# Performance work log

Measured on AMD Instinct MI355X. Metric: run time of the kernel, lower is better.

The kernel has to match this reference:

```python
import jax, jax.numpy as jnp
import numpy as np
import math

HEAD_SIZE = 64

def setup_inputs() -> dict:
    key = jax.random.key(0)
    k0, k1, k2, k3 = jax.random.split(key, 4)
    B, T, E, H = 4, 4096, 1024, HEAD_SIZE
    return {
        "x": jax.random.normal(k0, (B, T, E), dtype=jnp.float32),
        "Wq": jax.random.normal(k1, (E, H), dtype=jnp.float32) * (1.0 / math.sqrt(E)),
        "Wk": jax.random.normal(k2, (E, H), dtype=jnp.float32) * (1.0 / math.sqrt(E)),
        "Wv": jax.random.normal(k3, (E, H), dtype=jnp.float32) * (1.0 / math.sqrt(E)),
    }

def reference(x, Wq, Wk, Wv):
    # Single-head attention; faithful to source: softmax FIRST, then divide by sqrt(head_size)
    T = x.shape[-2]
    q = x @ Wq  # [B,T,H]
    k = x @ Wk
    v = x @ Wv
    scores = jnp.einsum('bth,bsh->bts', q, k)  # [B,T,T]
    # 'encoder' mask in this repo = lower-triangular (causal)
    causal = jnp.tril(jnp.ones((T, T), dtype=bool))
    scores = jnp.where(causal, scores, -jnp.inf)
    attn = jax.nn.softmax(scores, axis=-1) / jnp.sqrt(jnp.float32(q.shape[-1]))
    return jnp.einsum('bts,bsh->bth', attn, v)
```

## Files before the change

### kernel.cpp

```cpp
#include <hip/hip_runtime.h>
#include <math.h>

#define BB 4
#define TT 4096
#define EE 1024
#define HH 64

typedef __attribute__((ext_vector_type(8))) short bf16x8;
typedef _Float16 f16x8 __attribute__((ext_vector_type(8)));
typedef __attribute__((ext_vector_type(4))) float f32x4;

#define MFMA16(a, b, c)  __builtin_amdgcn_mfma_f32_16x16x32_bf16(a, b, c, 0, 0, 0)
#define MFMA16F(a, b, c) __builtin_amdgcn_mfma_f32_16x16x32_f16(a, b, c, 0, 0, 0)

__device__ __forceinline__ unsigned short f2bf_rne(float f) {
    unsigned u = __float_as_uint(f);
    unsigned r = u + 0x7fffu + ((u >> 16) & 1u);
    return (unsigned short)(r >> 16);
}
__device__ __forceinline__ float bf2f(unsigned short h) {
    return __uint_as_float(((unsigned)h) << 16);
}
__device__ __forceinline__ unsigned short f2h(float f) {
    union { _Float16 h; unsigned short u; } cv;
    cv.h = (_Float16)f;
    return cv.u;
}

__device__ __forceinline__ void async_copy16(const void* g, void* l) {
    __builtin_amdgcn_global_load_lds(
        (const __attribute__((address_space(1))) void*)g,
        (__attribute__((address_space(3))) void*)l, 16, 0, 0);
}
template<int N>
__device__ __forceinline__ void wait_vm() {
    __builtin_amdgcn_s_waitcnt(0x0f70 | (N & 15) | ((N >> 4) << 14));
}

__global__ __launch_bounds__(256) void wprep_kernel(
    const float* __restrict__ Wq, const float* __restrict__ Wk,
    const float* __restrict__ Wv,
    unsigned short* __restrict__ wt_hi, unsigned short* __restrict__ wt_lo)
{
    __shared__ float ts[64][65];
    const int which = blockIdx.x >> 4;
    const int e0 = (blockIdx.x & 15) * 64;
    const float* W = (which == 0) ? Wq : ((which == 1) ? Wk : Wv);
    const int t = threadIdx.x;
    const int h = t & 63;
    #pragma unroll
    for (int p = 0; p < 16; p++) {
        const int er = (t >> 6) + p * 4;
        ts[er][h] = W[(size_t)(e0 + er) * 64 + h];
    }
    __syncthreads();
    const int ew = t & 63;
    #pragma unroll
    for (int p = 0; p < 16; p++) {
        const int hh = (t >> 6) + p * 4;
        const float f = ts[ew][hh];
        const unsigned short hb = f2bf_rne(f);
        const unsigned short lb = f2bf_rne(f - bf2f(hb));
        const size_t o = (size_t)(which * 64 + hh) * 1024 + e0 + ew;
        wt_hi[o] = hb;
        wt_lo[o] = lb;
    }
}

__global__ __launch_bounds__(512) void proj_kernel(
    const float* __restrict__ x,
    const unsigned short* __restrict__ wt_hi, const unsigned short* __restrict__ wt_lo,
    unsigned short* __restrict__ qhf, unsigned short* __restrict__ qlf,
    unsigned short* __restrict__ kf, unsigned short* __restrict__ vt)
{
    __shared__ __align__(16) unsigned char smem[147456];
    const int tid = threadIdx.x;
    const int w = tid >> 6, lane = tid & 63;
    const int quad = lane >> 4, li = lane & 15;
    const int tg = w & 3, eh = w >> 2;
    const int row0 = (int)blockIdx.x * 64;
    const int tok = row0 + tg * 16 + li;
    const int s0 = ((int)blockIdx.x >> 3) & 15;

    f32x4 acc[12];
    #pragma unroll
    for (int mt = 0; mt < 12; mt++) acc[mt] = (f32x4){0.f, 0.f, 0.f, 0.f};

    const float* xr = x + (size_t)tok * EE + eh * 512 + quad * 8;

    const int r_l = lane >> 3, sl = lane & 7;
    const int cg = sl ^ r_l;
    const unsigned short* mat = (cg < 4) ? wt_hi : wt_lo;
    const int ce = (cg & 3) * 8;
    const int sA = (quad ^ (li & 7)) * 8;
    const int sB = ((4 + quad) ^ (li & 7)) * 8;

    auto dma_step = [&](int e0, unsigned char* dstbase) {
        #pragma unroll
        for (int ii = 0; ii < 6; ii++) {
            const int i = w * 6 + ii;
            const int ehc = i / 24;
            const int within = i % 24;
            const int row = within * 8 + r_l;
            const unsigned short* src = mat + (size_t)row * EE + ehc * 512 + e0 + ce;
            async_copy16(src, dstbase + ehc * 24576 + within * 1024);
        }
    };

    const int eo0 = ((s0 + 0) & 15) * 32;
    const int eo1 = ((s0 + 1) & 15) * 32;

    dma_step(eo0, smem);
    float4 fc0 = *(const float4*)(xr + eo0);
    float4 fc1 = *(const float4*)(xr + eo0 + 4);
    dma_step(eo1, smem + 49152);
    float4 fn0 = *(const float4*)(xr + eo1);
    float4 fn1 = *(const float4*)(xr + eo1 + 4);
    float4 ff0, ff1;

    for (int s = 0; s < 16; s++) {
        if (s + 2 < 16) {
            const int eo2 = ((s0 + s + 2) & 15) * 32;
            dma_step(eo2, smem + ((s + 2) % 3) * 49152);
            ff0 = *(const float4*)(xr + eo2);
            ff1 = *(const float4*)(xr + eo2 + 4);
            wait_vm<16>();
        } else if (s + 1 < 16) {
            wait_vm<8>();
        } else {
            wait_vm<0>();
        }
        __builtin_amdgcn_s_barrier();

        float fv[8] = {fc0.x, fc0.y, fc0.z, fc0.w, fc1.x, fc1.y, fc1.z, fc1.w};
        bf16x8 bh, bl;
        #pragma unroll
        for (int jj = 0; jj < 8; jj++) {
            unsigned short hb = f2bf_rne(fv[jj]);
            bh[jj] = (short)hb;
            bl[jj] = (short)f2bf_rne(fv[jj] - bf2f(hb));
        }
        const unsigned short* Wbase =
            (const unsigned short*)(smem + (s % 3) * 49152 + eh * 24576);
        #pragma unroll
        for (int mt = 0; mt < 12; mt++) {
            const unsigned short* rb = Wbase + (mt * 16 + li) * 64;
            bf16x8 Ah = *(const bf16x8*)(rb + sA);
            bf16x8 Al = *(const bf16x8*)(rb + sB);
            acc[mt] = MFMA16(Ah, bh, acc[mt]);
            acc[mt] = MFMA16(Ah, bl, acc[mt]);
            acc[mt] = MFMA16(Al, bh, acc[mt]);
        }
        __builtin_amdgcn_s_barrier();
        fc0 = fn0; fc1 = fn1; fn0 = ff0; fn1 = ff1;
    }

    float* Red = (float*)smem;
    if (eh == 1) {
        #pragma unroll
        for (int mt = 0; mt < 12; mt++)
            #pragma unroll
            for (int r = 0; r < 4; r++)
                Red[(size_t)(tg * 192 + mt * 16 + quad * 4 + r) * 17 + li] = acc[mt][r];
    }
    __syncthreads();
    if (eh == 0) {
        #pragma unroll
        for (int mt = 0; mt < 12; mt++)
            #pragma unroll
            for (int r = 0; r < 4; r++)
                acc[mt][r] += Red[(size_t)(tg * 192 + mt * 16 + quad * 4 + r) * 17 + li];
        const int bb = tok >> 12, tloc = tok & 4095;
        #pragma unroll
        for (int mt = 0; mt < 12; mt++) {
            if (mt < 4) {
                const int h = (mt & 3) * 16 + quad * 4;
                ushort4 hi4, lo4; float f; _Float16 hh;
                union { _Float16 h; unsigned short u; } cv;
                f = acc[mt][0]; hh = (_Float16)f; cv.h = hh; hi4.x = cv.u; lo4.x = f2h(f - (float)hh);
                f = acc[mt][1]; hh = (_Float16)f; cv.h = hh; hi4.y = cv.u; lo4.y = f2h(f - (float)hh);
                f = acc[mt][2]; hh = (_Float16)f; cv.h = hh; hi4.z = cv.u; lo4.z = f2h(f - (float)hh);
                f = acc[mt][3]; hh = (_Float16)f; cv.h = hh; hi4.w = cv.u; lo4.w = f2h(f - (float)hh);
                const size_t o = (size_t)tok * 64 + h;
                *(ushort4*)(qhf + o) = hi4;
                *(ushort4*)(qlf + o) = lo4;
            } else if (mt < 8) {
                const int h = (mt & 3) * 16 + quad * 4;
                ushort4 k4;
                k4.x = f2h(acc[mt][0]); k4.y = f2h(acc[mt][1]);
                k4.z = f2h(acc[mt][2]); k4.w = f2h(acc[mt][3]);
                *(ushort4*)(kf + (size_t)tok * 64 + h) = k4;
            } else {
                const int hv = (mt - 8) * 16 + quad * 4;
                #pragma unroll
                for (int r = 0; r < 4; r++)
                    vt[((size_t)(bb * 64 + hv + r) << 12) + tloc] = f2bf_rne(acc[mt][r]);
            }
        }
    }
}

__global__ __launch_bounds__(512) void flash_kernel(
    const unsigned short* __restrict__ qhf, const unsigned short* __restrict__ qlf,
    const unsigned short* __restrict__ kf,
    const unsigned short* __restrict__ vt, float* __restrict__ out)
{
    __shared__ __align__(16) unsigned char smem[89088];
    const int tid = threadIdx.x;
    const int w = tid >> 6, lane = tid & 63;
    const int quad = lane >> 4, li = lane & 15;
    const int lb = (int)blockIdx.x;
    const int b  = (lb & 7) >> 1;
    const int bx = ((lb >> 3) << 1) | (lb & 1);
    const float SM = 20.0f;

    const _Float16* kb = (const _Float16*)kf + ((size_t)b << 18);
    const unsigned short* vtb = vt + ((size_t)b << 18) + (size_t)li * 4096 + quad * 8;

    unsigned char* kbase = smem + w * 8192;
    unsigned short* PsA = (unsigned short*)(smem + 68608 + w * 2560);
    unsigned short* PsB = PsA + 640;
    float* Op = (float*)smem;
    float* Ml = (float*)(smem + 67584);

    const int r_l8 = lane >> 3, s8 = lane & 7;
    const int slf0 = ((quad)     ^ (li & 7)) * 8;
    const int slf1 = ((4 + quad) ^ (li & 7)) * 8;

    auto dma_tile = [&](int k0, unsigned char* dst) {
        #pragma unroll
        for (int i = 0; i < 4; i++) {
            const int row = i * 8 + r_l8;
            const int c = s8 ^ r_l8;
            async_copy16(kb + (size_t)(k0 + row) * 64 + c * 8, dst + i * 1024);
        }
    };

    #pragma unroll 1
    for (int phase = 0; phase < 2; phase++) {
        const int g = phase ? (127 - bx) : bx;
        const int q0 = g * 32;
        const int n_kt = g + 1;
        const int tok0 = q0 + li, tok1 = tok0 + 16;

        const size_t qo0 = ((size_t)(b << 12) + tok0) * 64 + quad * 8;
        const size_t qo1 = qo0 + 16 * 64;
        const _Float16* qh_p = (const _Float16*)qhf;
        const _Float16* ql_p = (const _Float16*)qlf;
        const f16x8 QhA0 = *(const f16x8*)(qh_p + qo0);
        const f16x8 QhA1 = *(const f16x8*)(qh_p + qo0 + 32);
        const f16x8 QlA0 = *(const f16x8*)(ql_p + qo0);
        const f16x8 QlA1 = *(const f16x8*)(ql_p + qo0 + 32);
        const f16x8 QhB0 = *(const f16x8*)(qh_p + qo1);
        const f16x8 QhB1 = *(const f16x8*)(qh_p + qo1 + 32);
        const f16x8 QlB0 = *(const f16x8*)(ql_p + qo1);
        const f16x8 QlB1 = *(const f16x8*)(ql_p + qo1 + 32);

        f32x4 accA[4], accB[4];
        #pragma unroll
        for (int mt = 0; mt < 4; mt++) {
            accA[mt] = (f32x4){0.f, 0.f, 0.f, 0.f};
            accB[mt] = (f32x4){0.f, 0.f, 0.f, 0.f};
        }
        float lA = 0.f, lB = 0.f;

        bf16x8 Vc[4], Vn[4];
        int bufp = 0;
        if (w < n_kt) {
            dma_tile(w * 32, kbase);
            #pragma unroll
            for (int hf = 0; hf < 4; hf++)
                Vc[hf] = *(const bf16x8*)(vtb + (size_t)hf * 65536 + w * 32);
        }

        for (int kt = w; kt < n_kt; kt += 8) {
            const int k0 = kt * 32;

            if (kt + 8 < n_kt) {
                dma_tile((kt + 8) * 32, kbase + (bufp ^ 1) * 4096);
                #pragma unroll
                for (int hf = 0; hf < 4; hf++)
                    Vn[hf] = *(const bf16x8*)(vtb + (size_t)hf * 65536 + (kt + 8) * 32);
                wait_vm<8>();
            } else {
                wait_vm<0>();
            }
            const _Float16* Kw = (const _Float16*)(kbase + bufp * 4096);

            f32x4 sA[2], sB[2];
            #pragma unroll
            for (int jf = 0; jf < 2; jf++) {
                const _Float16* rb = Kw + (jf * 16 + li) * 64;
                f16x8 K0 = *(const f16x8*)(rb + slf0);
                f16x8 K1 = *(const f16x8*)(rb + slf1);
                f32x4 a = (f32x4){0.f, 0.f, 0.f, 0.f};
                a = MFMA16F(K0, QhA0, a);
                a = MFMA16F(K1, QhA1, a);
                a = MFMA16F(K0, QlA0, a);
                a = MFMA16F(K1, QlA1, a);
                sA[jf] = a;
                f32x4 c2 = (f32x4){0.f, 0.f, 0.f, 0.f};
                c2 = MFMA16F(K0, QhB0, c2);
                c2 = MFMA16F(K1, QhB1, c2);
                c2 = MFMA16F(K0, QlB0, c2);
                c2 = MFMA16F(K1, QlB1, c2);
                sB[jf] = c2;
            }

            if (kt == n_kt - 1) {
                #pragma unroll
                for (int jf = 0; jf < 2; jf++)
                    #pragma unroll
                    for (int r = 0; r < 4; r++) {
                        const int j = k0 + jf * 16 + quad * 4 + r;
                        if (j > tok0) sA[jf][r] = -1e30f;
                        if (j > tok1) sB[jf][r] = -1e30f;
                    }
            }

            #pragma unroll
            for (int jf = 0; jf < 2; jf++)
                #pragma unroll
                for (int r = 0; r < 4; r++) {
                    sA[jf][r] = __expf(sA[jf][r] - SM); lA += sA[jf][r];
                    sB[jf][r] = __expf(sB[jf][r] - SM); lB += sB[jf][r];
                }

            #pragma unroll
            for (int jf = 0; jf < 2; jf++) {
                ushort4 pa, pb;
                pa.x = f2bf_rne(sA[jf][0]); pa.y = f2bf_rne(sA[jf][1]);
                pa.z = f2bf_rne(sA[jf][2]); pa.w = f2bf_rne(sA[jf][3]);
                pb.x = f2bf_rne(sB[jf][0]); pb.y = f2bf_rne(sB[jf][1]);
                pb.z = f2bf_rne(sB[jf][2]); pb.w = f2bf_rne(sB[jf][3]);
                *(ushort4*)&PsA[li * 40 + jf * 16 + quad * 4] = pa;
                *(ushort4*)&PsB[li * 40 + jf * 16 + quad * 4] = pb;
            }
            const bf16x8 PA = *(const bf16x8*)&PsA[li * 40 + quad * 8];
            const bf16x8 PB = *(const bf16x8*)&PsB[li * 40 + quad * 8];

            #pragma unroll
            for (int hf = 0; hf < 4; hf++) {
                accA[hf] = MFMA16(Vc[hf], PA, accA[hf]);
                accB[hf] = MFMA16(Vc[hf], PB, accB[hf]);
            }
            #pragma unroll
            for (int hf = 0; hf < 4; hf++) Vc[hf] = Vn[hf];
            bufp ^= 1;
        }

        lA += __shfl_xor(lA, 16); lA += __shfl_xor(lA, 32);
        lB += __shfl_xor(lB, 16); lB += __shfl_xor(lB, 32);

        __syncthreads();
        #pragma unroll
        for (int mt = 0; mt < 4; mt++)
            #pragma unroll
            for (int r = 0; r < 4; r++) {
                Op[(size_t)w * 2112 + (mt * 16 + quad * 4 + r) * 33 + li]      = accA[mt][r];
                Op[(size_t)w * 2112 + (mt * 16 + quad * 4 + r) * 33 + li + 16] = accB[mt][r];
            }
        if (quad == 0) {
            Ml[w * 32 + li]      = lA;
            Ml[w * 32 + 16 + li] = lB;
        }
        __syncthreads();

        const int i  = tid >> 4;
        const int hc = (tid & 15) * 4;
        float l = 0.f;
        #pragma unroll
        for (int ww = 0; ww < 8; ww++) l += Ml[ww * 32 + i];
        const float inv = 1.0f / (l * 8.0f);
        float4 o = {0.f, 0.f, 0.f, 0.f};
        #pragma unroll
        for (int ww = 0; ww < 8; ww++) {
            const float* base = Op + (size_t)ww * 2112;
            o.x += base[(hc + 0) * 33 + i];
            o.y += base[(hc + 1) * 33 + i];
            o.z += base[(hc + 2) * 33 + i];
            o.w += base[(hc + 3) * 33 + i];
        }
        o.x *= inv; o.y *= inv; o.z *= inv; o.w *= inv;
        *(float4*)(out + ((size_t)(b << 12) + q0 + i) * 64 + hc) = o;
        __syncthreads();
    }
}

extern "C" void kernel_launch(void* const* d_in, const int* in_sizes, int n_in,
                              void* d_out, int out_size, void* d_ws, size_t ws_size,
                              hipStream_t stream)
{
    const float* x  = (const float*)d_in[0];
    const float* Wq = (const float*)d_in[1];
    const float* Wk = (const float*)d_in[2];
    const float* Wv = (const float*)d_in[3];
    float* out = (float*)d_out;

    const size_t n_tok = (size_t)BB * TT * HH;
    unsigned short* qhf = (unsigned short*)d_ws;
    unsigned short* qlf = qhf + n_tok;
    unsigned short* kf  = qlf + n_tok;
    unsigned short* vt  = kf + n_tok;
    unsigned short* wt_hi = vt + n_tok;
    unsigned short* wt_lo = wt_hi + 192 * 1024;

    wprep_kernel<<<48, 256, 0, stream>>>(Wq, Wk, Wv, wt_hi, wt_lo);
    proj_kernel<<<(BB * TT) / 64, 512, 0, stream>>>(x, wt_hi, wt_lo,
                                                    qhf, qlf, kf, vt);
    flash_kernel<<<256, 512, 0, stream>>>(qhf, qlf, kf, vt, out);
}
```

Baseline: 156.3 us.

## Fuse weight prep, projection and flash attention into one persistent kernel

Merges the three kernels into a single 256-block launch that uses atomic grid-wide barriers in global memory between the weight-prep, projection and attention phases. The aim is to remove two kernel launch gaps and the tail of each separate kernel. In exchange it adds spin-wait barriers, a memset launch, and requires all 256 blocks, each using large shared memory, to be resident at once. The barrier gives up after a spin limit, which could silently break correctness if residency is not reached.

Result: slower. 361.1 us (+131.1%).

```diff
diff --git a/kernel.cpp b/kernel.cpp
--- a/kernel.cpp
+++ b/kernel.cpp
@@ -37,353 +37,372 @@
     __builtin_amdgcn_s_waitcnt(0x0f70 | (N & 15) | ((N >> 4) << 14));
 }
 
-__global__ __launch_bounds__(256) void wprep_kernel(
+__device__ __forceinline__ void grid_barrier(unsigned* cell) {
+    __threadfence();
+    __syncthreads();
+    if (threadIdx.x == 0) {
+        __hip_atomic_fetch_add(cell, 1u, __ATOMIC_ACQ_REL, __HIP_MEMORY_SCOPE_AGENT);
+        unsigned spins = 0;
+        while (__hip_atomic_load(cell, __ATOMIC_ACQUIRE, __HIP_MEMORY_SCOPE_AGENT) < 256u) {
+            __builtin_amdgcn_s_sleep(8);
+            if (++spins > 500000u) break;
+        }
+    }
+    __syncthreads();
+    __threadfence();
+}
+
+__global__ __launch_bounds__(512) void fused_kernel(
+    const float* __restrict__ x,
     const float* __restrict__ Wq, const float* __restrict__ Wk,
     const float* __restrict__ Wv,
-    unsigned short* __restrict__ wt_hi, unsigned short* __restrict__ wt_lo)
-{
-    __shared__ float ts[64][65];
-    const int which = blockIdx.x >> 4;
-    const int e0 = (blockIdx.x & 15) * 64;
-    const float* W = (which == 0) ? Wq : ((which == 1) ? Wk : Wv);
-    const int t = threadIdx.x;
-    const int h = t & 63;
-    #pragma unroll
-    for (int p = 0; p < 16; p++) {
-        const int er = (t >> 6) + p * 4;
-        ts[er][h] = W[(size_t)(e0 + er) * 64 + h];
-    }
-    __syncthreads();
-    const int ew = t & 63;
-    #pragma unroll
-    for (int p = 0; p < 16; p++) {
-        const int hh = (t >> 6) + p * 4;
-        const float f = ts[ew][hh];
-        const unsigned short hb = f2bf_rne(f);
-        const unsigned short lb = f2bf_rne(f - bf2f(hb));
-        const size_t o = (size_t)(which * 64 + hh) * 1024 + e0 + ew;
-        wt_hi[o] = hb;
-        wt_lo[o] = lb;
-    }
-}
-
-__global__ __launch_bounds__(512) void proj_kernel(
-    const float* __restrict__ x,
-    const unsigned short* __restrict__ wt_hi, const unsigned short* __restrict__ wt_lo,
+    unsigned short* __restrict__ wt_hi, unsigned short* __restrict__ wt_lo,
     unsigned short* __restrict__ qhf, unsigned short* __restrict__ qlf,
-    unsigned short* __restrict__ kf, unsigned short* __restrict__ vt)
+    unsigned short* __restrict__ kf, unsigned short* __restrict__ vt,
+    float* __restrict__ out, unsigned* __restrict__ bar)
 {
     __shared__ __align__(16) unsigned char smem[147456];
     const int tid = threadIdx.x;
-    const int w = tid >> 6, lane = tid & 63;
-    const int quad = lane >> 4, li = lane & 15;
-    const int tg = w & 3, eh = w >> 2;
-    const int row0 = (int)blockIdx.x * 64;
-    const int tok = row0 + tg * 16 + li;
-    const int s0 = ((int)blockIdx.x >> 3) & 15;
-
-    f32x4 acc[12];
-    #pragma unroll
-    for (int mt = 0; mt < 12; mt++) acc[mt] = (f32x4){0.f, 0.f, 0.f, 0.f};
-
-    const float* xr = x + (size_t)tok * EE + eh * 512 + quad * 8;
-
-    const int r_l = lane >> 3, sl = lane & 7;
-    const int cg = sl ^ r_l;
-    const unsigned short* mat = (cg < 4) ? wt_hi : wt_lo;
-    const int ce = (cg & 3) * 8;
-    const int sA = (quad ^ (li & 7)) * 8;
-    const int sB = ((4 + quad) ^ (li & 7)) * 8;
-
-    auto dma_step = [&](int e0, unsigned char* dstbase) {
+    const int bid = (int)blockIdx.x;
+
+    if (bid < 48) {
+        float (*ts)[65] = (float (*)[65])smem;
+        const int which = bid >> 4;
+        const int e0 = (bid & 15) * 64;
+        const float* W = (which == 0) ? Wq : ((which == 1) ? Wk : Wv);
+        if (tid < 256) {
+            const int h = tid & 63;
+            #pragma unroll
+            for (int p = 0; p < 16; p++) {
+                const int er = (tid >> 6) + p * 4;
+                ts[er][h] = W[(size_t)(e0 + er) * 64 + h];
+            }
+        }
+        __syncthreads();
+        if (tid < 256) {
+            const int ew = tid & 63;
+            #pragma unroll
+            for (int p = 0; p < 16; p++) {
+                const int hh = (tid >> 6) + p * 4;
+                const float f = ts[ew][hh];
+                const unsigned short hb = f2bf_rne(f);
+                const unsigned short lb = f2bf_rne(f - bf2f(hb));
+                const size_t o = (size_t)(which * 64 + hh) * 1024 + e0 + ew;
+                wt_hi[o] = hb;
+                wt_lo[o] = lb;
+            }
+        }
+    }
+
+    grid_barrier(bar + 0);
+
+    {
+        const int w = tid >> 6, lane = tid & 63;
+        const int quad = lane >> 4, li = lane & 15;
+        const int tg = w & 3, eh = w >> 2;
+        const int row0 = bid * 64;
+        const int tok = row0 + tg * 16 + li;
+        const int s0 = (bid >> 3) & 15;
+
+        f32x4 acc[12];
         #pragma unroll
-        for (int ii = 0; ii < 6; ii++) {
-            const int i = w * 6 + ii;
-            const int ehc = i / 24;
-            const int within = i % 24;
-            const int row = within * 8 + r_l;
-            const unsigned short* src = mat + (size_t)row * EE + ehc * 512 + e0 + ce;
-            async_copy16(src, dstbase + ehc * 24576 + within * 1024);
-        }
-    };
-
-    const int eo0 = ((s0 + 0) & 15) * 32;
-    const int eo1 = ((s0 + 1) & 15) * 32;
-
-    dma_step(eo0, smem);
-    float4 fc0 = *(const float4*)(xr + eo0);
-    float4 fc1 = *(const float4*)(xr + eo0 + 4);
-    dma_step(eo1, smem + 49152);
-    float4 fn0 = *(const float4*)(xr + eo1);
-    float4 fn1 = *(const float4*)(xr + eo1 + 4);
-    float4 ff0, ff1;
-
-    for (int s = 0; s < 16; s++) {
-        if (s + 2 < 16) {
-            const int eo2 = ((s0 + s + 2) & 15) * 32;
-            dma_step(eo2, smem + ((s + 2) % 3) * 49152);
-            ff0 = *(const float4*)(xr + eo2);
-            ff1 = *(const float4*)(xr + eo2 + 4);
-            wait_vm<16>();
-        } else if (s + 1 < 16) {
-            wait_vm<8>();
-        } else {
-            wait_vm<0>();
-        }
-        __builtin_amdgcn_s_barrier();
-
-        float fv[8] = {fc0.x, fc0.y, fc0.z, fc0.w, fc1.x, fc1.y, fc1.z, fc1.w};
-        bf16x8 bh, bl;
-        #pragma unroll
-        for (int jj = 0; jj < 8; jj++) {
-            unsigned short hb = f2bf_rne(fv[jj]);
-            bh[jj] = (short)hb;
-            bl[jj] = (short)f2bf_rne(fv[jj] - bf2f(hb));
-        }
-        const unsigned short* Wbase =
-            (const unsigned short*)(smem + (s % 3) * 49152 + eh * 24576);
-        #pragma unroll
-        for (int mt = 0; mt < 12; mt++) {
-            const unsigned short* rb = Wbase + (mt * 16 + li) * 64;
-            bf16x8 Ah = *(const bf16x8*)(rb + sA);
-            bf16x8 Al = *(const bf16x8*)(rb + sB);
-            acc[mt] = MFMA16(Ah, bh, acc[mt]);
-            acc[mt] = MFMA16(Ah, bl, acc[mt]);
-            acc[mt] = MFMA16(Al, bh, acc[mt]);
-        }
-        __builtin_amdgcn_s_barrier();
-        fc0 = fn0; fc1 = fn1; fn0 = ff0; fn1 = ff1;
-    }
-
-    float* Red = (float*)smem;
-    if (eh == 1) {
-        #pragma unroll
-        for (int mt = 0; mt < 12; mt++)
-            #pragma unroll
-            for (int r = 0; r < 4; r++)
-                Red[(size_t)(tg * 192 + mt * 16 + quad * 4 + r) * 17 + li] = acc[mt][r];
-    }
-    __syncthreads();
-    if (eh == 0) {
-        #pragma unroll
-        for (int mt = 0; mt < 12; mt++)
-            #pragma unroll
-            for (int r = 0; r < 4; r++)
-                acc[mt][r] += Red[(size_t)(tg * 192 + mt * 16 + quad * 4 + r) * 17 + li];
-        const int bb = tok >> 12, tloc = tok & 4095;
-        #pragma unroll
-        for (int mt = 0; mt < 12; mt++) {
-            if (mt < 4) {
-                const int h = (mt & 3) * 16 + quad * 4;
-                ushort4 hi4, lo4; float f; _Float16 hh;
-                union { _Float16 h; unsigned short u; } cv;
-                f = acc[mt][0]; hh = (_Float16)f; cv.h = hh; hi4.x = cv.u; lo4.x = f2h(f - (float)hh);
-                f = acc[mt][1]; hh = (_Float16)f; cv.h = hh; hi4.y = cv.u; lo4.y = f2h(f - (float)hh);
-                f = acc[mt][2]; hh = (_Float16)f; cv.h = hh; hi4.z = cv.u; lo4.z = f2h(f - (float)hh);
-                f = acc[mt][3]; hh = (_Float16)f; cv.h = hh; hi4.w = cv.u; lo4.w = f2h(f - (float)hh);
-                const size_t o = (size_t)tok * 64 + h;
-                *(ushort4*)(qhf + o) = hi4;
-                *(ushort4*)(qlf + o) = lo4;
-            } else if (mt < 8) {
-                const int h = (mt & 3) * 16 + quad * 4;
-                ushort4 k4;
-                k4.x = f2h(acc[mt][0]); k4.y = f2h(acc[mt][1]);
-                k4.z = f2h(acc[mt][2]); k4.w = f2h(acc[mt][3]);
-                *(ushort4*)(kf + (size_t)tok * 64 + h) = k4;
-            } else {
-                const int hv = (mt - 8) * 16 + quad * 4;
-                #pragma unroll
-                for (int r = 0; r < 4; r++)
-                    vt[((size_t)(bb * 64 + hv + r) << 12) + tloc] = f2bf_rne(acc[mt][r]);
-            }
-        }
-    }
-}
-
-__global__ __launch_bounds__(512) void flash_kernel(
-    const unsigned short* __restrict__ qhf, const unsigned short* __restrict__ qlf,
-    const unsigned short* __restrict__ kf,
-    const unsigned short* __restrict__ vt, float* __restrict__ out)
-{
-    __shared__ __align__(16) unsigned char smem[89088];
-    const int tid = threadIdx.x;
-    const int w = tid >> 6, lane = tid & 63;
-    const int quad = lane >> 4, li = lane & 15;
-    const int lb = (int)blockIdx.x;
-    const int b  = (lb & 7) >> 1;
-    const int bx = ((lb >> 3) << 1) | (lb & 1);
-    const float SM = 20.0f;
-
-    const _Float16* kb = (const _Float16*)kf + ((size_t)b << 18);
-    const unsigned short* vtb = vt + ((size_t)b << 18) + (size_t)li * 4096 + quad * 8;
-
-    unsigned char* kbase = smem + w * 8192;
-    unsigned short* PsA = (unsigned short*)(smem + 68608 + w * 2560);
-    unsigned short* PsB = PsA + 640;
-    float* Op = (float*)smem;
-    float* Ml = (float*)(smem + 67584);
-
-    const int r_l8 = lane >> 3, s8 = lane & 7;
-    const int slf0 = ((quad)     ^ (li & 7)) * 8;
-    const int slf1 = ((4 + quad) ^ (li & 7)) * 8;
-
-    auto dma_tile = [&](int k0, unsigned char* dst) {
-        #pragma unroll
-        for (int i = 0; i < 4; i++) {
-            const int row = i * 8 + r_l8;
-            const int c = s8 ^ r_l8;
-            async_copy16(kb + (size_t)(k0 + row) * 64 + c * 8, dst + i * 1024);
-        }
-    };
-
-    #pragma unroll 1
-    for (int phase = 0; phase < 2; phase++) {
-        const int g = phase ? (127 - bx) : bx;
-        const int q0 = g * 32;
-        const int n_kt = g + 1;
-        const int tok0 = q0 + li, tok1 = tok0 + 16;
-
-        const size_t qo0 = ((size_t)(b << 12) + tok0) * 64 + quad * 8;
-        const size_t qo1 = qo0 + 16 * 64;
-        const _Float16* qh_p = (const _Float16*)qhf;
-        const _Float16* ql_p = (const _Float16*)qlf;
-        const f16x8 QhA0 = *(const f16x8*)(qh_p + qo0);
-        const f16x8 QhA1 = *(const f16x8*)(qh_p + qo0 + 32);
-        const f16x8 QlA0 = *(const f16x8*)(ql_p + qo0);
-        const f16x8 QlA1 = *(const f16x8*)(ql_p + qo0 + 32);
-        const f16x8 QhB0 = *(const f16x8*)(qh_p + qo1);
-        const f16x8 QhB1 = *(const f16x8*)(qh_p + qo1 + 32);
-        const f16x8 QlB0 = *(const f16x8*)(ql_p + qo1);
-        const f16x8 QlB1 = *(const f16x8*)(ql_p + qo1 + 32);
-
-        f32x4 accA[4], accB[4];
-        #pragma unroll
-        for (int mt = 0; mt < 4; mt++) {
-            accA[mt] = (f32x4){0.f, 0.f, 0.f, 0.f};
-            accB[mt] = (f32x4){0.f, 0.f, 0.f, 0.f};
-        }
-        float lA = 0.f, lB = 0.f;
-
-        bf16x8 Vc[4], Vn[4];
-        int bufp = 0;
-        if (w < n_kt) {
-            dma_tile(w * 32, kbase);
-            #pragma unroll
-            for (int hf = 0; hf < 4; hf++)
-                Vc[hf] = *(const bf16x8*)(vtb + (size_t)hf * 65536 + w * 32);
-        }
-
-        for (int kt = w; kt < n_kt; kt += 8) {
-            const int k0 = kt * 32;
-
-            if (kt + 8 < n_kt) {
-                dma_tile((kt + 8) * 32, kbase + (bufp ^ 1) * 4096);
-                #pragma unroll
-                for (int hf = 0; hf < 4; hf++)
-                    Vn[hf] = *(const bf16x8*)(vtb + (size_t)hf * 65536 + (kt + 8) * 32);
+        for (int mt = 0; mt < 12; mt++) acc[mt] = (f32x4){0.f, 0.f, 0.f, 0.f};
+
+        const float* xr = x + (size_t)tok * EE + eh * 512 + quad * 8;
+
+        const int r_l = lane >> 3, sl = lane & 7;
+        const int cg = sl ^ r_l;
+        const unsigned short* mat = (cg < 4) ? wt_hi : wt_lo;
+        const int ce = (cg & 3) * 8;
+        const int sA = (quad ^ (li & 7)) * 8;
+        const int sB = ((4 + quad) ^ (li & 7)) * 8;
+
+        auto dma_step = [&](int e0, unsigned char* dstbase) {
+            #pragma unroll
+            for (int ii = 0; ii < 6; ii++) {
+                const int i = w * 6 + ii;
+                const int ehc = i / 24;
+                const int within = i % 24;
+                const int row = within * 8 + r_l;
+                const unsigned short* src = mat + (size_t)row * EE + ehc * 512 + e0 + ce;
+                async_copy16(src, dstbase + ehc * 24576 + within * 1024);
+            }
+        };
+
+        const int eo0 = ((s0 + 0) & 15) * 32;
+        const int eo1 = ((s0 + 1) & 15) * 32;
+
+        dma_step(eo0, smem);
+        float4 fc0 = *(const float4*)(xr + eo0);
+        float4 fc1 = *(const float4*)(xr + eo0 + 4);
+        dma_step(eo1, smem + 49152);
+        float4 fn0 = *(const float4*)(xr + eo1);
+        float4 fn1 = *(const float4*)(xr + eo1 + 4);
+        float4 ff0, ff1;
+
+        for (int s = 0; s < 16; s++) {
+            if (s + 2 < 16) {
+                const int eo2 = ((s0 + s + 2) & 15) * 32;
+                dma_step(eo2, smem + ((s + 2) % 3) * 49152);
+                ff0 = *(const float4*)(xr + eo2);
+                ff1 = *(const float4*)(xr + eo2 + 4);
+                wait_vm<16>();
+            } else if (s + 1 < 16) {
                 wait_vm<8>();
             } else {
                 wait_vm<0>();
             }
-            const _Float16* Kw = (const _Float16*)(kbase + bufp * 4096);
-
-            f32x4 sA[2], sB[2];
-            #pragma unroll
-            for (int jf = 0; jf < 2; jf++) {
-                const _Float16* rb = Kw + (jf * 16 + li) * 64;
-                f16x8 K0 = *(const f16x8*)(rb + slf0);
-                f16x8 K1 = *(const f16x8*)(rb + slf1);
-                f32x4 a = (f32x4){0.f, 0.f, 0.f, 0.f};
-                a = MFMA16F(K0, QhA0, a);
-                a = MFMA16F(K1, QhA1, a);
-                a = MFMA16F(K0, QlA0, a);
-                a = MFMA16F(K1, QlA1, a);
-                sA[jf] = a;
-                f32x4 c2 = (f32x4){0.f, 0.f, 0.f, 0.f};
-                c2 = MFMA16F(K0, QhB0, c2);
-                c2 = MFMA16F(K1, QhB1, c2);
-                c2 = MFMA16F(K0, QlB0, c2);
-                c2 = MFMA16F(K1, QlB1, c2);
-                sB[jf] = c2;
-            }
-
-            if (kt == n_kt - 1) {
+            __builtin_amdgcn_s_barrier();
+
+            float fv[8] = {fc0.x, fc0.y, fc0.z, fc0.w, fc1.x, fc1.y, fc1.z, fc1.w};
+            bf16x8 bh, bl;
+            #pragma unroll
+            for (int jj = 0; jj < 8; jj++) {
+                unsigned short hb = f2bf_rne(fv[jj]);
+                bh[jj] = (short)hb;
+                bl[jj] = (short)f2bf_rne(fv[jj] - bf2f(hb));
+            }
+            const unsigned short* Wbase =
+                (const unsigned short*)(smem + (s % 3) * 49152 + eh * 24576);
+            #pragma unroll
+            for (int mt = 0; mt < 12; mt++) {
+                const unsigned short* rb = Wbase + (mt * 16 + li) * 64;
+                bf16x8 Ah = *(const bf16x8*)(rb + sA);
+                bf16x8 Al = *(const bf16x8*)(rb + sB);
+                acc[mt] = MFMA16(Ah, bh, acc[mt]);
+                acc[mt] = MFMA16(Ah, bl, acc[mt]);
+                acc[mt] = MFMA16(Al, bh, acc[mt]);
+            }
+            __builtin_amdgcn_s_barrier();
+            fc0 = fn0; fc1 = fn1; fn0 = ff0; fn1 = ff1;
+        }
+
+        float* Red = (float*)smem;
+        if (eh == 1) {
+            #pragma unroll
+            for (int mt = 0; mt < 12; mt++)
+                #pragma unroll
+                for (int r = 0; r < 4; r++)
+                    Red[(size_t)(tg * 192 + mt * 16 + quad * 4 + r) * 17 + li] = acc[mt][r];
+        }
+        __syncthreads();
+        if (eh == 0) {
+            #pragma unroll
+            for (int mt = 0; mt < 12; mt++)
+                #pragma unroll
+                for (int r = 0; r < 4; r++)
+                    acc[mt][r] += Red[(size_t)(tg * 192 + mt * 16 + quad * 4 + r) * 17 + li];
+            const int bb = tok >> 12, tloc = tok & 4095;
+            #pragma unroll
+            for (int mt = 0; mt < 12; mt++) {
+                if (mt < 4) {
+                    const int h = (mt & 3) * 16 + quad * 4;
+                    ushort4 hi4, lo4; float f; _Float16 hh;
+                    union { _Float16 h; unsigned short u; } cv;
+                    f = acc[mt][0]; hh = (_Float16)f; cv.h = hh; hi4.x = cv.u; lo4.x = f2h(f - (float)hh);
+                    f = acc[mt][1]; hh = (_Float16)f; cv.h = hh; hi4.y = cv.u; lo4.y = f2h(f - (float)hh);
+                    f = acc[mt][2]; hh = (_Float16)f; cv.h = hh; hi4.z = cv.u; lo4.z = f2h(f - (float)hh);
+                    f = acc[mt][3]; hh = (_Float16)f; cv.h = hh; hi4.w = cv.u; lo4.w = f2h(f - (float)hh);
+                    const size_t o = (size_t)tok * 64 + h;
+                    *(ushort4*)(qhf + o) = hi4;
+                    *(ushort4*)(qlf + o) = lo4;
+                } else if (mt < 8) {
+                    const int h = (mt & 3) * 16 + quad * 4;
+                    ushort4 k4;
+                    k4.x = f2h(acc[mt][0]); k4.y = f2h(acc[mt][1]);
+                    k4.z = f2h(acc[mt][2]); k4.w = f2h(acc[mt][3]);
+                    *(ushort4*)(kf + (size_t)tok * 64 + h) = k4;
+                } else {
+                    const int hv = (mt - 8) * 16 + quad * 4;
+                    #pragma unroll
+                    for (int r = 0; r < 4; r++)
+                        vt[((size_t)(bb * 64 + hv + r) << 12) + tloc] = f2bf_rne(acc[mt][r]);
+                }
+            }
+        }
+    }
+
+    grid_barrier(bar + 1);
+
+    {
+        const int w = tid >> 6, lane = tid & 63;
+        const int quad = lane >> 4, li = lane & 15;
+        const int lb = bid;
+        const int b  = (lb & 7) >> 1;
+        const int bx = ((lb >> 3) << 1) | (lb & 1);
+        const float SM = 20.0f;
+
+        const _Float16* kb = (const _Float16*)kf + ((size_t)b << 18);
+        const unsigned short* vtb = vt + ((size_t)b << 18) + (size_t)li * 4096 + quad * 8;
+
+        unsigned char* kbase = smem + w * 8192;
+        unsigned short* PsA = (unsigned short*)(smem + 68608 + w * 2560);
+        unsigned short* PsB = PsA + 640;
+        float* Op = (float*)smem;
+        float* Ml = (float*)(smem + 67584);
+
+        const int r_l8 = lane >> 3, s8 = lane & 7;
+        const int slf0 = ((quad)     ^ (li & 7)) * 8;
+        const int slf1 = ((4 + quad) ^ (li & 7)) * 8;
+
+        auto dma_tile = [&](int k0, unsigned char* dst) {
+            #pragma unroll
+            for (int i = 0; i < 4; i++) {
+                const int row = i * 8 + r_l8;
+                const int c = s8 ^ r_l8;
+                async_copy16(kb + (size_t)(k0 + row) * 64 + c * 8, dst + i * 1024);
+            }
+        };
+
+        #pragma unroll 1
+        for (int phase = 0; phase < 2; phase++) {
+            const int g = phase ? (127 - bx) : bx;
+            const int q0 = g * 32;
+            const int n_kt = g + 1;
+            const int tok0 = q0 + li, tok1 = tok0 + 16;
+
+            const size_t qo0 = ((size_t)(b << 12) + tok0) * 64 + quad * 8;
+            const size_t qo1 = qo0 + 16 * 64;
+            const _Float16* qh_p = (const _Float16*)qhf;
+            const _Float16* ql_p = (const _Float16*)qlf;
+            const f16x8 QhA0 = *(const f16x8*)(qh_p + qo0);
+            const f16x8 QhA1 = *(const f16x8*)(qh_p + qo0 + 32);
+            const f16x8 QlA0 = *(const f16x8*)(ql_p + qo0);
+            const f16x8 QlA1 = *(const f16x8*)(ql_p + qo0 + 32);
+            const f16x8 QhB0 = *(const f16x8*)(qh_p + qo1);
+            const f16x8 QhB1 = *(const f16x8*)(qh_p + qo1 + 32);
+            const f16x8 QlB0 = *(const f16x8*)(ql_p + qo1);
+            const f16x8 QlB1 = *(const f16x8*)(ql_p + qo1 + 32);
+
+            f32x4 accA[4], accB[4];
+            #pragma unroll
+            for (int mt = 0; mt < 4; mt++) {
+                accA[mt] = (f32x4){0.f, 0.f, 0.f, 0.f};
+                accB[mt] = (f32x4){0.f, 0.f, 0.f, 0.f};
+            }
+            float lA = 0.f, lB = 0.f;
+
+            bf16x8 Vc[4], Vn[4];
+            int bufp = 0;
+            if (w < n_kt) {
+                dma_tile(w * 32, kbase);
+                #pragma unroll
+                for (int hf = 0; hf < 4; hf++)
+                    Vc[hf] = *(const bf16x8*)(vtb + (size_t)hf * 65536 + w * 32);
+            }
+
+            for (int kt = w; kt < n_kt; kt += 8) {
+                const int k0 = kt * 32;
+
+                if (kt + 8 < n_kt) {
+                    dma_tile((kt + 8) * 32, kbase + (bufp ^ 1) * 4096);
+                    #pragma unroll
+                    for (int hf = 0; hf < 4; hf++)
+                        Vn[hf] = *(const bf16x8*)(vtb + (size_t)hf * 65536 + (kt + 8) * 32);
+                    wait_vm<8>();
+                } else {
+                    wait_vm<0>();
+                }
+                const _Float16* Kw = (const _Float16*)(kbase + bufp * 4096);
+
+                f32x4 sA[2], sB[2];
+                #pragma unroll
+                for (int jf = 0; jf < 2; jf++) {
+                    const _Float16* rb = Kw + (jf * 16 + li) * 64;
+                    f16x8 K0 = *(const f16x8*)(rb + slf0);
+                    f16x8 K1 = *(const f16x8*)(rb + slf1);
+                    f32x4 a = (f32x4){0.f, 0.f, 0.f, 0.f};
+                    a = MFMA16F(K0, QhA0, a);
+                    a = MFMA16F(K1, QhA1, a);
+                    a = MFMA16F(K0, QlA0, a);
+                    a = MFMA16F(K1, QlA1, a);
+                    sA[jf] = a;
+                    f32x4 c2 = (f32x4){0.f, 0.f, 0.f, 0.f};
+                    c2 = MFMA16F(K0, QhB0, c2);
+                    c2 = MFMA16F(K1, QhB1, c2);
+                    c2 = MFMA16F(K0, QlB0, c2);
+                    c2 = MFMA16F(K1, QlB1, c2);
+                    sB[jf] = c2;
+                }
+
+                if (kt == n_kt - 1) {
+                    #pragma unroll
+                    for (int jf = 0; jf < 2; jf++)
+                        #pragma unroll
+                        for (int r = 0; r < 4; r++) {
+                            const int j = k0 + jf * 16 + quad * 4 + r;
+                            if (j > tok0) sA[jf][r] = -1e30f;
+                            if (j > tok1) sB[jf][r] = -1e30f;
+                        }
+                }
+
                 #pragma unroll
                 for (int jf = 0; jf < 2; jf++)
                     #pragma unroll
                     for (int r = 0; r < 4; r++) {
-                        const int j = k0 + jf * 16 + quad * 4 + r;
-                        if (j > tok0) sA[jf][r] = -1e30f;
-                        if (j > tok1) sB[jf][r] = -1e30f;
+                        sA[jf][r] = __expf(sA[jf][r] - SM); lA += sA[jf][r];
+                        sB[jf][r] = __expf(sB[jf][r] - SM); lB += sB[jf][r];
                     }
-            }
-
-            #pragma unroll
-            for (int jf = 0; jf < 2; jf++)
+
+                #pragma unroll
+                for (int jf = 0; jf < 2; jf++) {
+                    ushort4 pa, pb;
+                    pa.x = f2bf_rne(sA[jf][0]); pa.y = f2bf_rne(sA[jf][1]);
+                    pa.z = f2bf_rne(sA[jf][2]); pa.w = f2bf_rne(sA[jf][3]);
+                    pb.x = f2bf_rne(sB[jf][0]); pb.y = f2bf_rne(sB[jf][1]);
+                    pb.z = f2bf_rne(sB[jf][2]); pb.w = f2bf_rne(sB[jf][3]);
+                    *(ushort4*)&PsA[li * 40 + jf * 16 + quad * 4] = pa;
+                    *(ushort4*)&PsB[li * 40 + jf * 16 + quad * 4] = pb;
+                }
+                const bf16x8 PA = *(const bf16x8*)&PsA[li * 40 + quad * 8];
+                const bf16x8 PB = *(const bf16x8*)&PsB[li * 40 + quad * 8];
+
+                #pragma unroll
+                for (int hf = 0; hf < 4; hf++) {
+                    accA[hf] = MFMA16(Vc[hf], PA, accA[hf]);
+                    accB[hf] = MFMA16(Vc[hf], PB, accB[hf]);
+                }
+                #pragma unroll
+                for (int hf = 0; hf < 4; hf++) Vc[hf] = Vn[hf];
+                bufp ^= 1;
+            }
+
+            lA += __shfl_xor(lA, 16); lA += __shfl_xor(lA, 32);
+            lB += __shfl_xor(lB, 16); lB += __shfl_xor(lB, 32);
+
+            __syncthreads();
+            #pragma unroll
+            for (int mt = 0; mt < 4; mt++)
                 #pragma unroll
                 for (int r = 0; r < 4; r++) {
-                    sA[jf][r] = __expf(sA[jf][r] - SM); lA += sA[jf][r];
-                    sB[jf][r] = __expf(sB[jf][r] - SM); lB += sB[jf][r];
-                }
-
-            #pragma unroll
-            for (int jf = 0; jf < 2; jf++) {
-                ushort4 pa, pb;
-                pa.x = f2bf_rne(sA[jf][0]); pa.y = f2bf_rne(sA[jf][1]);
-                pa.z = f2bf_rne(sA[jf][2]); pa.w = f2bf_rne(sA[jf][3]);
-                pb.x = f2bf_rne(sB[jf][0]); pb.y = f2bf_rne(sB[jf][1]);
-                pb.z = f2bf_rne(sB[jf][2]); pb.w = f2bf_rne(sB[jf][3]);
-                *(ushort4*)&PsA[li * 40 + jf * 16 + quad * 4] = pa;
-                *(ushort4*)&PsB[li * 40 + jf * 16 + quad * 4] = pb;
-            }
-            const bf16x8 PA = *(const bf16x8*)&PsA[li * 40 + quad * 8];
-            const bf16x8 PB = *(const bf16x8*)&PsB[li * 40 + quad * 8];
-
-            #pragma unroll
-            for (int hf = 0; hf < 4; hf++) {
-                accA[hf] = MFMA16(Vc[hf], PA, accA[hf]);
-                accB[hf] = MFMA16(Vc[hf], PB, accB[hf]);
-            }
-            #pragma unroll
-            for (int hf = 0; hf < 4; hf++) Vc[hf] = Vn[hf];
-            bufp ^= 1;
-        }
-
-        lA += __shfl_xor(lA, 16); lA += __shfl_xor(lA, 32);
-        lB += __shfl_xor(lB, 16); lB += __shfl_xor(lB, 32);
-
-        __syncthreads();
-        #pragma unroll
-        for (int mt = 0; mt < 4; mt++)
-            #pragma unroll
-            for (int r = 0; r < 4; r++) {
-                Op[(size_t)w * 2112 + (mt * 16 + quad * 4 + r) * 33 + li]      = accA[mt][r];
-                Op[(size_t)w * 2112 + (mt * 16 + quad * 4 + r) * 33 + li + 16] = accB[mt][r];
-            }
-        if (quad == 0) {
-            Ml[w * 32 + li]      = lA;
-            Ml[w * 32 + 16 + li] = lB;
-        }
-        __syncthreads();
-
-        const int i  = tid >> 4;
-        const int hc = (tid & 15) * 4;
-        float l = 0.f;
-        #pragma unroll
-        for (int ww = 0; ww < 8; ww++) l += Ml[ww * 32 + i];
-        const float inv = 1.0f / (l * 8.0f);
-        float4 o = {0.f, 0.f, 0.f, 0.f};
-        #pragma unroll
-        for (int ww = 0; ww < 8; ww++) {
-            const float* base = Op + (size_t)ww * 2112;
-            o.x += base[(hc + 0) * 33 + i];
-            o.y += base[(hc + 1) * 33 + i];
-            o.z += base[(hc + 2) * 33 + i];
-            o.w += base[(hc + 3) * 33 + i];
-        }
-        o.x *= inv; o.y *= inv; o.z *= inv; o.w *= inv;
-        *(float4*)(out + ((size_t)(b << 12) + q0 + i) * 64 + hc) = o;
-        __syncthreads();
+                    Op[(size_t)w * 2112 + (mt * 16 + quad * 4 + r) * 33 + li]      = accA[mt][r];
+                    Op[(size_t)w * 2112 + (mt * 16 + quad * 4 + r) * 33 + li + 16] = accB[mt][r];
+                }
+            if (quad == 0) {
+                Ml[w * 32 + li]      = lA;
+                Ml[w * 32 + 16 + li] = lB;
+            }
+            __syncthreads();
+
+            const int i  = tid >> 4;
+            const int hc = (tid & 15) * 4;
+            float l = 0.f;
+            #pragma unroll
+            for (int ww = 0; ww < 8; ww++) l += Ml[ww * 32 + i];
+            const float inv = 1.0f / (l * 8.0f);
+            float4 o = {0.f, 0.f, 0.f, 0.f};
+            #pragma unroll
+            for (int ww = 0; ww < 8; ww++) {
+                const float* base = Op + (size_t)ww * 2112;
+                o.x += base[(hc + 0) * 33 + i];
+                o.y += base[(hc + 1) * 33 + i];
+                o.z += base[(hc + 2) * 33 + i];
+                o.w += base[(hc + 3) * 33 + i];
+            }
+            o.x *= inv; o.y *= inv; o.z *= inv; o.w *= inv;
+            *(float4*)(out + ((size_t)(b << 12) + q0 + i) * 64 + hc) = o;
+            __syncthreads();
+        }
     }
 }
 
@@ -404,9 +423,9 @@
     unsigned short* vt  = kf + n_tok;
     unsigned short* wt_hi = vt + n_tok;
     unsigned short* wt_lo = wt_hi + 192 * 1024;
-
-    wprep_kernel<<<48, 256, 0, stream>>>(Wq, Wk, Wv, wt_hi, wt_lo);
-    proj_kernel<<<(BB * TT) / 64, 512, 0, stream>>>(x, wt_hi, wt_lo,
-                                                    qhf, qlf, kf, vt);
-    flash_kernel<<<256, 512, 0, stream>>>(qhf, qlf, kf, vt, out);
-}
+    unsigned* bar = (unsigned*)(wt_lo + 192 * 1024);
+
+    hipMemsetAsync(bar, 0, 8, stream);
+    fused_kernel<<<256, 512, 0, stream>>>(x, Wq, Wk, Wv, wt_hi, wt_lo,
+                                          qhf, qlf, kf, vt, out, bar);
+}
```
